# Performance work log

Measured on AMD Instinct MI355X. Metric: run time of the kernel, lower is better.

The kernel has to match this reference:

```python
import jax, jax.numpy as jnp
import numpy as np

B, O, GRID = 2048, 48, 112
SIGMA = 5.0


def setup_inputs() -> dict:
    key = jax.random.key(0)
    k1, k2, k3, k4, k5 = jax.random.split(key, 5)
    s = float(GRID - 1)
    xL = jax.random.uniform(k1, (B,), dtype=jnp.float32) * s
    yL = jax.random.uniform(k2, (B,), dtype=jnp.float32) * s
    obj_list = jax.random.uniform(k3, (B, O, 2), dtype=jnp.float32) * s
    obj_num = jax.random.randint(k4, (B,), 0, O + 1, dtype=jnp.int32)
    road_mask = jax.random.randint(k5, (B, GRID, GRID), 0, 2, dtype=jnp.int32)
    return {"xL": xL, "yL": yL, "obj_list": obj_list, "obj_num": obj_num,
            "road_mask": road_mask, "H": GRID, "W": GRID}


def reference(xL, yL, obj_list, obj_num, road_mask, H, W):
    # Faithful vectorization of batch_gaussian_tensor_obj.
    # exp(-(dx^2+dy^2)/(2s^2)) is separable: exp(-dx^2/..) * exp(-dy^2/..),
    # so per-object splats reduce to a batched matmul over the object axis.
    inv = 1.0 / (2.0 * SIGMA * SIGMA)
    x = jnp.arange(H, dtype=jnp.float32)  # row coordinate grid
    y = jnp.arange(W, dtype=jnp.float32)  # col coordinate grid

    # positive goal gaussian, rank-1 outer product per batch element
    gx = jnp.exp(-((x[None, :] - xL[:, None]) ** 2) * inv)  # [B,H]
    gy = jnp.exp(-((y[None, :] - yL[:, None]) ** 2) * inv)  # [B,W]
    goal = gx[:, :, None] * gy[:, None, :]                   # [B,H,W]

    # negative object gaussians; note original swaps xy: xo=xy[1], yo=xy[0]
    xo = obj_list[:, :, 1]  # [B,O] row coords
    yo = obj_list[:, :, 0]  # [B,O] col coords
    ex = jnp.exp(-((x[None, None, :] - xo[:, :, None]) ** 2) * inv)  # [B,O,H]
    ey = jnp.exp(-((y[None, None, :] - yo[:, :, None]) ** 2) * inv)  # [B,O,W]
    valid = (jnp.arange(O)[None, :] < obj_num[:, None]).astype(jnp.float32)  # [B,O]
    obj = jnp.einsum('boh,bow->bhw', ex * valid[:, :, None], ey)     # [B,H,W]

    channel = 0.5 + 0.5 * goal - 0.5 * obj
    channel = jnp.where(road_mask == 0, 0.0, channel)
    return channel
```

## Files before the change

kernel.cpp:

```cpp
#include <hip/hip_runtime.h>

#define GRID_N 112
#define O_MAX 48
#define HW_N (GRID_N * GRID_N)
#define NT 448

typedef _Float16 half8 __attribute__((ext_vector_type(8)));
typedef float    f32x4 __attribute__((ext_vector_type(4)));

__global__ __launch_bounds__(NT) void goalmap_kernel(
    const float* __restrict__ xL, const float* __restrict__ yL,
    const float* __restrict__ obj_list, const int* __restrict__ obj_num,
    const int* __restrict__ road_mask, float* __restrict__ out)
{
    constexpr float INV = 1.0f / (2.0f * 5.0f * 5.0f);

    const int b   = blockIdx.x;
    const int tid = threadIdx.x;
    const int lane = tid & 63;
    const int wid  = tid >> 6;
    const int m    = lane & 15;
    const int quad = lane >> 4;

    const int n  = obj_num[b];
    const float xl = xL[b];
    const float yl = yL[b];
    const float* ob = obj_list + (size_t)b * (O_MAX * 2);
    const int*   rm = road_mask + (size_t)b * HW_N;
    float*       op = out       + (size_t)b * HW_N;

    float ax0[8], ay0[8], ax1[8], ay1[8];
    #pragma unroll
    for (int j = 0; j < 8; ++j) {
        int k = quad * 8 + j;
        ax0[j] = ob[k * 2 + 1];
        ay0[j] = ob[k * 2];
        bool g = (k + 32 < n);
        ax1[j] = g ? ob[(k + 32) * 2 + 1] : 0.f;
        ay1[j] = g ? ob[(k + 32) * 2]     : 0.f;
    }
    __builtin_amdgcn_sched_barrier(0);

    int mpf[7][4];
    const int h0 = wid * 16 + quad * 4;
    #pragma unroll
    for (int i = 0; i < 7; ++i) {
        int base = h0 * GRID_N + i * 16 + m;
        #pragma unroll
        for (int r = 0; r < 4; ++r)
            mpf[i][r] = rm[base + r * GRID_N];
    }
    __builtin_amdgcn_sched_barrier(0);

    const int ksteps = (n >= 32) ? 2 : 1;

    const float fh = (float)(wid * 16 + m);
    half8 a0, a1;
    #pragma unroll
    for (int j = 0; j < 8; ++j) {
        int k = quad * 8 + j;
        float val = 0.f;
        if (k <= n) {
            float cx = (k < n) ? ax0[j] : xl;
            float s  = (k < n) ? -0.5f  : 0.5f;
            float d  = fh - cx;
            val = s * __expf(-d * d * INV);
        }
        a0[j] = (_Float16)val;
    }
    if (ksteps == 2) {
        #pragma unroll
        for (int j = 0; j < 8; ++j) {
            int k = quad * 8 + j + 32;
            float val = 0.f;
            if (k <= n) {
                float cx = (k < n) ? ax1[j] : xl;
                float s  = (k < n) ? -0.5f  : 0.5f;
                float d  = fh - cx;
                val = s * __expf(-d * d * INV);
            }
            a1[j] = (_Float16)val;
        }
    }

    #pragma unroll
    for (int tw = 0; tw < 7; ++tw) {
        const float fw = (float)(tw * 16 + m);
        half8 b0;
        #pragma unroll
        for (int j = 0; j < 8; ++j) {
            int k = quad * 8 + j;
            float val = 0.f;
            if (k <= n) {
                float cy = (k < n) ? ay0[j] : yl;
                float d  = fw - cy;
                val = __expf(-d * d * INV);
            }
            b0[j] = (_Float16)val;
        }
        f32x4 acc = {0.f, 0.f, 0.f, 0.f};
        acc = __builtin_amdgcn_mfma_f32_16x16x32_f16(a0, b0, acc, 0, 0, 0);
        if (ksteps == 2) {
            half8 b1;
            #pragma unroll
            for (int j = 0; j < 8; ++j) {
                int k = quad * 8 + j + 32;
                float val = 0.f;
                if (k <= n) {
                    float cy = (k < n) ? ay1[j] : yl;
                    float d  = fw - cy;
                    val = __expf(-d * d * INV);
                }
                b1[j] = (_Float16)val;
            }
            acc = __builtin_amdgcn_mfma_f32_16x16x32_f16(a1, b1, acc, 0, 0, 0);
        }

        const int w0 = tw * 16 + m;
        #pragma unroll
        for (int r = 0; r < 4; ++r) {
            float v = 0.5f + acc[r];
            v = (mpf[tw][r] == 0) ? 0.f : v;
            op[(h0 + r) * GRID_N + w0] = v;
        }
    }
}

extern "C" void kernel_launch(void* const* d_in, const int* in_sizes, int n_in,
                              void* d_out, int out_size, void* d_ws, size_t ws_size,
                              hipStream_t stream) {
    const float* xL        = (const float*)d_in[0];
    const float* yL        = (const float*)d_in[1];
    const float* obj_list  = (const float*)d_in[2];
    const int*   obj_num   = (const int*)d_in[3];
    const int*   road_mask = (const int*)d_in[4];
    float*       out       = (float*)d_out;
    const int B = in_sizes[0];

    goalmap_kernel<<<B, NT, 0, stream>>>(xL, yL, obj_list, obj_num, road_mask, out);
}
```

Measured before the change: 208.4 us.

## Stage MFMA results through LDS for coalesced 16-byte mask loads and output stores

Swaps the MFMA operand order so each lane's accumulator holds four consecutive columns, writes the tile to shared memory, then reads it back in a linear layout. Road-mask loads and output stores become contiguous 128-bit vector accesses per wave instead of scattered 4-byte column accesses. Object coordinates are also loaded as float2 pairs. The cost is 50 KB of LDS per block, which may limit occupancy, plus an extra LDS round trip.

```diff
diff --git a/kernel.cpp b/kernel.cpp
--- a/kernel.cpp
+++ b/kernel.cpp
@@ -4,9 +4,12 @@
 #define O_MAX 48
 #define HW_N (GRID_N * GRID_N)
 #define NT 448
+#define SDW (16 * GRID_N)
 
 typedef _Float16 half8 __attribute__((ext_vector_type(8)));
 typedef float    f32x4 __attribute__((ext_vector_type(4)));
+typedef float    f32x2 __attribute__((ext_vector_type(2)));
+typedef int      i32x4 __attribute__((ext_vector_type(4)));
 
 __global__ __launch_bounds__(NT) void goalmap_kernel(
     const float* __restrict__ xL, const float* __restrict__ yL,
@@ -15,8 +18,10 @@
 {
     constexpr float INV = 1.0f / (2.0f * 5.0f * 5.0f);
 
-    const int b   = blockIdx.x;
-    const int tid = threadIdx.x;
+    __shared__ float lds[7][SDW];
+
+    const int b    = blockIdx.x;
+    const int tid  = threadIdx.x;
     const int lane = tid & 63;
     const int wid  = tid >> 6;
     const int m    = lane & 15;
@@ -26,30 +31,25 @@
     const float xl = xL[b];
     const float yl = yL[b];
     const float* ob = obj_list + (size_t)b * (O_MAX * 2);
-    const int*   rm = road_mask + (size_t)b * HW_N;
-    float*       op = out       + (size_t)b * HW_N;
+    const int*   rm = road_mask + (size_t)b * HW_N + wid * SDW;
+    float*       op = out       + (size_t)b * HW_N + wid * SDW;
 
-    float ax0[8], ay0[8], ax1[8], ay1[8];
+    f32x2 oc0[8], oc1[8];
     #pragma unroll
     for (int j = 0; j < 8; ++j) {
         int k = quad * 8 + j;
-        ax0[j] = ob[k * 2 + 1];
-        ay0[j] = ob[k * 2];
+        oc0[j] = *(const f32x2*)&ob[k * 2];
         bool g = (k + 32 < n);
-        ax1[j] = g ? ob[(k + 32) * 2 + 1] : 0.f;
-        ay1[j] = g ? ob[(k + 32) * 2]     : 0.f;
+        f32x2 z = {0.f, 0.f};
+        oc1[j] = g ? *(const f32x2*)&ob[(k + 32) * 2] : z;
     }
     __builtin_amdgcn_sched_barrier(0);
 
-    int mpf[7][4];
-    const int h0 = wid * 16 + quad * 4;
+    i32x4 mk[7];
+    const int ldw = lane * 4;
     #pragma unroll
-    for (int i = 0; i < 7; ++i) {
-        int base = h0 * GRID_N + i * 16 + m;
-        #pragma unroll
-        for (int r = 0; r < 4; ++r)
-            mpf[i][r] = rm[base + r * GRID_N];
-    }
+    for (int i = 0; i < 7; ++i)
+        mk[i] = *(const i32x4*)&rm[i * 256 + ldw];
     __builtin_amdgcn_sched_barrier(0);
 
     const int ksteps = (n >= 32) ? 2 : 1;
@@ -61,7 +61,7 @@
         int k = quad * 8 + j;
         float val = 0.f;
         if (k <= n) {
-            float cx = (k < n) ? ax0[j] : xl;
+            float cx = (k < n) ? oc0[j][1] : xl;
             float s  = (k < n) ? -0.5f  : 0.5f;
             float d  = fh - cx;
             val = s * __expf(-d * d * INV);
@@ -74,7 +74,7 @@
             int k = quad * 8 + j + 32;
             float val = 0.f;
             if (k <= n) {
-                float cx = (k < n) ? ax1[j] : xl;
+                float cx = (k < n) ? oc1[j][1] : xl;
                 float s  = (k < n) ? -0.5f  : 0.5f;
                 float d  = fh - cx;
                 val = s * __expf(-d * d * INV);
@@ -86,43 +86,47 @@
     #pragma unroll
     for (int tw = 0; tw < 7; ++tw) {
         const float fw = (float)(tw * 16 + m);
-        half8 b0;
+        half8 e0;
         #pragma unroll
         for (int j = 0; j < 8; ++j) {
             int k = quad * 8 + j;
             float val = 0.f;
             if (k <= n) {
-                float cy = (k < n) ? ay0[j] : yl;
+                float cy = (k < n) ? oc0[j][0] : yl;
                 float d  = fw - cy;
                 val = __expf(-d * d * INV);
             }
-            b0[j] = (_Float16)val;
+            e0[j] = (_Float16)val;
         }
         f32x4 acc = {0.f, 0.f, 0.f, 0.f};
-        acc = __builtin_amdgcn_mfma_f32_16x16x32_f16(a0, b0, acc, 0, 0, 0);
+        acc = __builtin_amdgcn_mfma_f32_16x16x32_f16(e0, a0, acc, 0, 0, 0);
         if (ksteps == 2) {
-            half8 b1;
+            half8 e1;
             #pragma unroll
             for (int j = 0; j < 8; ++j) {
                 int k = quad * 8 + j + 32;
                 float val = 0.f;
                 if (k <= n) {
-                    float cy = (k < n) ? ay1[j] : yl;
+                    float cy = (k < n) ? oc1[j][0] : yl;
                     float d  = fw - cy;
                     val = __expf(-d * d * INV);
                 }
-                b1[j] = (_Float16)val;
+                e1[j] = (_Float16)val;
             }
-            acc = __builtin_amdgcn_mfma_f32_16x16x32_f16(a1, b1, acc, 0, 0, 0);
+            acc = __builtin_amdgcn_mfma_f32_16x16x32_f16(e1, a1, acc, 0, 0, 0);
         }
+        *(f32x4*)&lds[wid][m * GRID_N + tw * 16 + quad * 4] = acc;
+    }
 
-        const int w0 = tw * 16 + m;
+    #pragma unroll
+    for (int i = 0; i < 7; ++i) {
+        f32x4 v = *(const f32x4*)&lds[wid][i * 256 + ldw];
+        i32x4 mm = mk[i];
+        f32x4 o;
         #pragma unroll
-        for (int r = 0; r < 4; ++r) {
-            float v = 0.5f + acc[r];
-            v = (mpf[tw][r] == 0) ? 0.f : v;
-            op[(h0 + r) * GRID_N + w0] = v;
-        }
+        for (int j = 0; j < 4; ++j)
+            o[j] = (mm[j] == 0) ? 0.f : (0.5f + v[j]);
+        *(f32x4*)&op[i * 256 + ldw] = o;
     }
 }
 
```

Result: faster. 197.1 us (-5.5%).

## Process two batch elements per block and prefetch second element's object coordinates

Applied to the files above, without the earlier changes.

Each block now handles two batch elements in sequence, cutting the grid in half. The second element's object coordinates are gathered before the first element is computed, so that load latency overlaps with compute. Object coordinates are now read as paired float2 loads instead of two scalar loads. The second element's road mask is still loaded only after the first sweep, and the block count drops to 1024, which may lower occupancy and latency hiding.

```diff
diff --git a/kernel.cpp b/kernel.cpp
--- a/kernel.cpp
+++ b/kernel.cpp
@@ -4,64 +4,46 @@
 #define O_MAX 48
 #define HW_N (GRID_N * GRID_N)
 #define NT 448
+#define NB 2
 
 typedef _Float16 half8 __attribute__((ext_vector_type(8)));
 typedef float    f32x4 __attribute__((ext_vector_type(4)));
+typedef float    f32x2 __attribute__((ext_vector_type(2)));
 
-__global__ __launch_bounds__(NT) void goalmap_kernel(
-    const float* __restrict__ xL, const float* __restrict__ yL,
-    const float* __restrict__ obj_list, const int* __restrict__ obj_num,
-    const int* __restrict__ road_mask, float* __restrict__ out)
-{
-    constexpr float INV = 1.0f / (2.0f * 5.0f * 5.0f);
+constexpr float INV = 1.0f / (2.0f * 5.0f * 5.0f);
 
-    const int b   = blockIdx.x;
-    const int tid = threadIdx.x;
-    const int lane = tid & 63;
-    const int wid  = tid >> 6;
-    const int m    = lane & 15;
-    const int quad = lane >> 4;
-
-    const int n  = obj_num[b];
-    const float xl = xL[b];
-    const float yl = yL[b];
-    const float* ob = obj_list + (size_t)b * (O_MAX * 2);
-    const int*   rm = road_mask + (size_t)b * HW_N;
-    float*       op = out       + (size_t)b * HW_N;
-
-    float ax0[8], ay0[8], ax1[8], ay1[8];
+__device__ __forceinline__ void gather_oc(const float* __restrict__ ob, int n, int quad,
+                                          f32x2* oc0, f32x2* oc1) {
     #pragma unroll
     for (int j = 0; j < 8; ++j) {
         int k = quad * 8 + j;
-        ax0[j] = ob[k * 2 + 1];
-        ay0[j] = ob[k * 2];
+        oc0[j] = *(const f32x2*)&ob[k * 2];
         bool g = (k + 32 < n);
-        ax1[j] = g ? ob[(k + 32) * 2 + 1] : 0.f;
-        ay1[j] = g ? ob[(k + 32) * 2]     : 0.f;
+        f32x2 z = {0.f, 0.f};
+        oc1[j] = g ? *(const f32x2*)&ob[(k + 32) * 2] : z;
     }
-    __builtin_amdgcn_sched_barrier(0);
+}
 
-    int mpf[7][4];
-    const int h0 = wid * 16 + quad * 4;
+__device__ __forceinline__ void load_masks(const int* __restrict__ rm, int h0, int m,
+                                           int (*mk)[4]) {
     #pragma unroll
     for (int i = 0; i < 7; ++i) {
         int base = h0 * GRID_N + i * 16 + m;
         #pragma unroll
         for (int r = 0; r < 4; ++r)
-            mpf[i][r] = rm[base + r * GRID_N];
+            mk[i][r] = rm[base + r * GRID_N];
     }
-    __builtin_amdgcn_sched_barrier(0);
+}
 
-    const int ksteps = (n >= 32) ? 2 : 1;
-
-    const float fh = (float)(wid * 16 + m);
-    half8 a0, a1;
+__device__ __forceinline__ void build_a(int n, int ksteps, float fh, float xl, int quad,
+                                        const f32x2* oc0, const f32x2* oc1,
+                                        half8& a0, half8& a1) {
     #pragma unroll
     for (int j = 0; j < 8; ++j) {
         int k = quad * 8 + j;
         float val = 0.f;
         if (k <= n) {
-            float cx = (k < n) ? ax0[j] : xl;
+            float cx = (k < n) ? oc0[j][1] : xl;
             float s  = (k < n) ? -0.5f  : 0.5f;
             float d  = fh - cx;
             val = s * __expf(-d * d * INV);
@@ -74,7 +56,7 @@
             int k = quad * 8 + j + 32;
             float val = 0.f;
             if (k <= n) {
-                float cx = (k < n) ? ax1[j] : xl;
+                float cx = (k < n) ? oc1[j][1] : xl;
                 float s  = (k < n) ? -0.5f  : 0.5f;
                 float d  = fh - cx;
                 val = s * __expf(-d * d * INV);
@@ -82,7 +64,12 @@
             a1[j] = (_Float16)val;
         }
     }
+}
 
+__device__ __forceinline__ void sweep(int n, int ksteps, float yl, int m, int quad, int h0,
+                                      const f32x2* oc0, const f32x2* oc1,
+                                      half8 a0, half8 a1, const int (*mk)[4],
+                                      float* __restrict__ op) {
     #pragma unroll
     for (int tw = 0; tw < 7; ++tw) {
         const float fw = (float)(tw * 16 + m);
@@ -92,7 +79,7 @@
             int k = quad * 8 + j;
             float val = 0.f;
             if (k <= n) {
-                float cy = (k < n) ? ay0[j] : yl;
+                float cy = (k < n) ? oc0[j][0] : yl;
                 float d  = fw - cy;
                 val = __expf(-d * d * INV);
             }
@@ -107,7 +94,7 @@
                 int k = quad * 8 + j + 32;
                 float val = 0.f;
                 if (k <= n) {
-                    float cy = (k < n) ? ay1[j] : yl;
+                    float cy = (k < n) ? oc1[j][0] : yl;
                     float d  = fw - cy;
                     val = __expf(-d * d * INV);
                 }
@@ -115,14 +102,74 @@
             }
             acc = __builtin_amdgcn_mfma_f32_16x16x32_f16(a1, b1, acc, 0, 0, 0);
         }
-
         const int w0 = tw * 16 + m;
         #pragma unroll
         for (int r = 0; r < 4; ++r) {
             float v = 0.5f + acc[r];
-            v = (mpf[tw][r] == 0) ? 0.f : v;
+            v = (mk[tw][r] == 0) ? 0.f : v;
             op[(h0 + r) * GRID_N + w0] = v;
         }
+    }
+}
+
+__global__ __launch_bounds__(NT) void goalmap_kernel(
+    const float* __restrict__ xL, const float* __restrict__ yL,
+    const float* __restrict__ obj_list, const int* __restrict__ obj_num,
+    const int* __restrict__ road_mask, float* __restrict__ out, int B)
+{
+    const int tid  = threadIdx.x;
+    const int lane = tid & 63;
+    const int wid  = tid >> 6;
+    const int m    = lane & 15;
+    const int quad = lane >> 4;
+    const int h0   = wid * 16 + quad * 4;
+    const float fh = (float)(wid * 16 + m);
+
+    const int b0 = blockIdx.x * NB;
+    const int b1 = b0 + 1;
+
+    const int   n0  = obj_num[b0];
+    const float xl0 = xL[b0], yl0 = yL[b0];
+    const int ksteps0 = (n0 >= 32) ? 2 : 1;
+
+    f32x2 oc0_b0[8], oc1_b0[8];
+    gather_oc(obj_list + (size_t)b0 * (O_MAX * 2), n0, quad, oc0_b0, oc1_b0);
+    __builtin_amdgcn_sched_barrier(0);
+
+    int mk0[7][4];
+    load_masks(road_mask + (size_t)b0 * HW_N, h0, m, mk0);
+    __builtin_amdgcn_sched_barrier(0);
+
+    f32x2 oc0_b1[8], oc1_b1[8];
+    int n1 = 0; float xl1 = 0.f, yl1 = 0.f;
+    const bool has_b1 = (b1 < B);
+    if (has_b1) {
+        n1 = obj_num[b1]; xl1 = xL[b1]; yl1 = yL[b1];
+        gather_oc(obj_list + (size_t)b1 * (O_MAX * 2), n1, quad, oc0_b1, oc1_b1);
+    }
+    __builtin_amdgcn_sched_barrier(0);
+
+    half8 a0_b0, a1_b0;
+    build_a(n0, ksteps0, fh, xl0, quad, oc0_b0, oc1_b0, a0_b0, a1_b0);
+    __builtin_amdgcn_sched_barrier(0);
+
+    sweep(n0, ksteps0, yl0, m, quad, h0, oc0_b0, oc1_b0, a0_b0, a1_b0, mk0,
+          out + (size_t)b0 * HW_N);
+    __builtin_amdgcn_sched_barrier(0);
+
+    if (has_b1) {
+        const int ksteps1 = (n1 >= 32) ? 2 : 1;
+
+        int mk1[7][4];
+        load_masks(road_mask + (size_t)b1 * HW_N, h0, m, mk1);
+        __builtin_amdgcn_sched_barrier(0);
+
+        half8 a0_b1, a1_b1;
+        build_a(n1, ksteps1, fh, xl1, quad, oc0_b1, oc1_b1, a0_b1, a1_b1);
+        __builtin_amdgcn_sched_barrier(0);
+
+        sweep(n1, ksteps1, yl1, m, quad, h0, oc0_b1, oc1_b1, a0_b1, a1_b1, mk1,
+              out + (size_t)b1 * HW_N);
     }
 }
 
@@ -137,5 +184,6 @@
     float*       out       = (float*)d_out;
     const int B = in_sizes[0];
 
-    goalmap_kernel<<<B, NT, 0, stream>>>(xL, yL, obj_list, obj_num, road_mask, out);
+    const int grid = (B + NB - 1) / NB;
+    goalmap_kernel<<<grid, NT, 0, stream>>>(xL, yL, obj_list, obj_num, road_mask, out, B);
 }
```

After: 210.6 us. About the same (+1.0%).

## Pack road mask into bitmask in prepass kernel before goal-map compute

Applied to the files above, without the earlier changes.

Adds a separate pre-pass kernel that reads the int32 road mask in 32-byte vector chunks and packs it into one bit per cell in workspace. The main kernel then reads bytes and extracts its bit instead of loading an int per output element, and object coordinates are loaded as float2 pairs. Total mask traffic is not reduced, since the full int mask is still read plus a packed write and re-read, and a second launch is added. The main gain sought is more coalesced vector reads of the mask versus the strided per-lane int loads before.

```diff
diff --git a/kernel.cpp b/kernel.cpp
--- a/kernel.cpp
+++ b/kernel.cpp
@@ -4,53 +4,69 @@
 #define O_MAX 48
 #define HW_N (GRID_N * GRID_N)
 #define NT 448
+#define PKB (HW_N / 8)
 
 typedef _Float16 half8 __attribute__((ext_vector_type(8)));
 typedef float    f32x4 __attribute__((ext_vector_type(4)));
+typedef float    f32x2 __attribute__((ext_vector_type(2)));
+typedef int      i32x4 __attribute__((ext_vector_type(4)));
+
+constexpr float INV = 1.0f / (2.0f * 5.0f * 5.0f);
+
+__global__ __launch_bounds__(256) void pack_mask(
+    const int* __restrict__ rm, unsigned char* __restrict__ pk, int total8)
+{
+    const int idx    = blockIdx.x * 256 + threadIdx.x;
+    const int stride = gridDim.x * 256;
+    for (int i = idx; i < total8; i += stride) {
+        const i32x4* p = (const i32x4*)(rm + (size_t)i * 8);
+        i32x4 a = p[0], b = p[1];
+        unsigned c = 0;
+        c |= (a[0] != 0) ? 1u   : 0u;  c |= (a[1] != 0) ? 2u   : 0u;
+        c |= (a[2] != 0) ? 4u   : 0u;  c |= (a[3] != 0) ? 8u   : 0u;
+        c |= (b[0] != 0) ? 16u  : 0u;  c |= (b[1] != 0) ? 32u  : 0u;
+        c |= (b[2] != 0) ? 64u  : 0u;  c |= (b[3] != 0) ? 128u : 0u;
+        pk[i] = (unsigned char)c;
+    }
+}
 
 __global__ __launch_bounds__(NT) void goalmap_kernel(
     const float* __restrict__ xL, const float* __restrict__ yL,
     const float* __restrict__ obj_list, const int* __restrict__ obj_num,
-    const int* __restrict__ road_mask, float* __restrict__ out)
+    const unsigned char* __restrict__ pk, float* __restrict__ out)
 {
-    constexpr float INV = 1.0f / (2.0f * 5.0f * 5.0f);
-
-    const int b   = blockIdx.x;
-    const int tid = threadIdx.x;
+    const int b    = blockIdx.x;
+    const int tid  = threadIdx.x;
     const int lane = tid & 63;
     const int wid  = tid >> 6;
     const int m    = lane & 15;
     const int quad = lane >> 4;
+    const int h0   = wid * 16 + quad * 4;
 
     const int n  = obj_num[b];
     const float xl = xL[b];
     const float yl = yL[b];
     const float* ob = obj_list + (size_t)b * (O_MAX * 2);
-    const int*   rm = road_mask + (size_t)b * HW_N;
-    float*       op = out       + (size_t)b * HW_N;
+    float*       op = out      + (size_t)b * HW_N;
 
-    float ax0[8], ay0[8], ax1[8], ay1[8];
+    const unsigned char* pb = pk + (size_t)b * PKB;
+    const int cb = m >> 3;
+    unsigned mb[7][4];
+    #pragma unroll
+    for (int tw = 0; tw < 7; ++tw)
+        #pragma unroll
+        for (int r = 0; r < 4; ++r)
+            mb[tw][r] = pb[(h0 + r) * 14 + tw * 2 + cb];
+    const int bitpos = m & 7;
+
+    f32x2 oc0[8], oc1[8];
     #pragma unroll
     for (int j = 0; j < 8; ++j) {
         int k = quad * 8 + j;
-        ax0[j] = ob[k * 2 + 1];
-        ay0[j] = ob[k * 2];
-        bool g = (k + 32 < n);
-        ax1[j] = g ? ob[(k + 32) * 2 + 1] : 0.f;
-        ay1[j] = g ? ob[(k + 32) * 2]     : 0.f;
+        oc0[j] = *(const f32x2*)&ob[k * 2];
+        f32x2 z = {0.f, 0.f};
+        oc1[j] = (k + 32 < O_MAX) ? *(const f32x2*)&ob[(k + 32) * 2] : z;
     }
-    __builtin_amdgcn_sched_barrier(0);
-
-    int mpf[7][4];
-    const int h0 = wid * 16 + quad * 4;
-    #pragma unroll
-    for (int i = 0; i < 7; ++i) {
-        int base = h0 * GRID_N + i * 16 + m;
-        #pragma unroll
-        for (int r = 0; r < 4; ++r)
-            mpf[i][r] = rm[base + r * GRID_N];
-    }
-    __builtin_amdgcn_sched_barrier(0);
 
     const int ksteps = (n >= 32) ? 2 : 1;
 
@@ -61,7 +77,7 @@
         int k = quad * 8 + j;
         float val = 0.f;
         if (k <= n) {
-            float cx = (k < n) ? ax0[j] : xl;
+            float cx = (k < n) ? oc0[j][1] : xl;
             float s  = (k < n) ? -0.5f  : 0.5f;
             float d  = fh - cx;
             val = s * __expf(-d * d * INV);
@@ -74,7 +90,7 @@
             int k = quad * 8 + j + 32;
             float val = 0.f;
             if (k <= n) {
-                float cx = (k < n) ? ax1[j] : xl;
+                float cx = (k < n) ? oc1[j][1] : xl;
                 float s  = (k < n) ? -0.5f  : 0.5f;
                 float d  = fh - cx;
                 val = s * __expf(-d * d * INV);
@@ -92,7 +108,7 @@
             int k = quad * 8 + j;
             float val = 0.f;
             if (k <= n) {
-                float cy = (k < n) ? ay0[j] : yl;
+                float cy = (k < n) ? oc0[j][0] : yl;
                 float d  = fw - cy;
                 val = __expf(-d * d * INV);
             }
@@ -107,7 +123,7 @@
                 int k = quad * 8 + j + 32;
                 float val = 0.f;
                 if (k <= n) {
-                    float cy = (k < n) ? ay1[j] : yl;
+                    float cy = (k < n) ? oc1[j][0] : yl;
                     float d  = fw - cy;
                     val = __expf(-d * d * INV);
                 }
@@ -115,12 +131,11 @@
             }
             acc = __builtin_amdgcn_mfma_f32_16x16x32_f16(a1, b1, acc, 0, 0, 0);
         }
-
         const int w0 = tw * 16 + m;
         #pragma unroll
         for (int r = 0; r < 4; ++r) {
             float v = 0.5f + acc[r];
-            v = (mpf[tw][r] == 0) ? 0.f : v;
+            v = ((mb[tw][r] >> bitpos) & 1u) ? v : 0.f;
             op[(h0 + r) * GRID_N + w0] = v;
         }
     }
@@ -137,5 +152,9 @@
     float*       out       = (float*)d_out;
     const int B = in_sizes[0];
 
-    goalmap_kernel<<<B, NT, 0, stream>>>(xL, yL, obj_list, obj_num, road_mask, out);
+    unsigned char* pk = (unsigned char*)d_ws;
+    const int total8 = B * PKB;
+
+    pack_mask<<<2048, 256, 0, stream>>>(road_mask, pk, total8);
+    goalmap_kernel<<<B, NT, 0, stream>>>(xL, yL, obj_list, obj_num, pk, out);
 }
```

Measured after the change: 221.0 us. 1.06x slower.
